# Kernel optimization log

Hardware: AMD Instinct MI355X
Metric: run time of the kernel (lower is better)

Reference implementation:

```python
import jax, jax.numpy as jnp
import numpy as np

N = 8192
IN, HID, NH, TOT = 64, 64, 4, 128
DH = TOT // NH  # 32


def setup_inputs() -> dict:
    key = jax.random.key(0)
    ks = jax.random.split(key, 8)
    s = 0.05
    return {
        "input": jax.random.normal(ks[0], (N, IN), jnp.float32),
        "hx": jax.random.normal(ks[1], (N, HID), jnp.float32),
        "Wq": jax.random.normal(ks[2], (NH, TOT, DH), jnp.float32) * s,
        "Wk": jax.random.normal(ks[3], (NH, TOT, DH), jnp.float32) * s,
        "Wr": jax.random.normal(ks[4], (TOT, HID), jnp.float32) * s,
        "br": jnp.zeros((HID,), jnp.float32),
        "Wz": jax.random.normal(ks[5], (TOT, HID), jnp.float32) * s,
        "bz": jnp.zeros((HID,), jnp.float32),
        "Wh": jax.random.normal(ks[6], (TOT, HID), jnp.float32) * s,
        "bh": jnp.zeros((HID,), jnp.float32),
    }


def _dyn_adj(x, Wq, Wk):
    # x: [N, T]; multi-head attention adjacency, averaged over heads -> [N, N]
    q = jnp.einsum('nt,htd->hnd', x, Wq)
    k = jnp.einsum('nt,htd->hnd', x, Wk)
    scores = jnp.einsum('hnd,hmd->hnm', q, k) / jnp.sqrt(jnp.float32(DH))
    return jnp.mean(jax.nn.softmax(scores, axis=-1), axis=0)  # [N, N]


def reference(input, hx, Wq, Wk, Wr, br, Wz, bz, Wh, bh):
    x = jnp.concatenate([input, hx], axis=1)          # [N, TOT]
    adj = _dyn_adj(x, Wq, Wk)                         # [N, N] row-stochastic
    ax = adj @ x                                      # shared adjacency application
    r = jax.nn.sigmoid(ax @ Wr + br)                  # [N, HID]
    z = jax.nn.sigmoid(ax @ Wz + bz)                  # [N, HID]
    x2 = jnp.concatenate([input, r * hx], axis=1)     # [N, TOT]
    h = jnp.tanh((adj @ x2) @ Wh + bh)                # [N, HID]
    return z * hx + (1.0 - z) * h
```

## Files before the change

kernel.cpp:

```cpp
#include <hip/hip_runtime.h>
#include <hip/hip_bf16.h>

#define NN 8192
#define TOTD 128
#define HIDD 64
#define NHEAD 4
#define DHD 32
#define NCQ 16
#define JPB (NN / 32 / NCQ)

typedef __attribute__((ext_vector_type(8))) short short8;
typedef __attribute__((ext_vector_type(4))) float f32x4;
typedef __attribute__((ext_vector_type(16))) float f32x16;

__device__ __forceinline__ short f2b(float f) {
  unsigned u = __builtin_bit_cast(unsigned, f);
  u += 0x7fff + ((u >> 16) & 1);
  return (short)(u >> 16);
}
__device__ __forceinline__ short f2b_fast(float f) {
  unsigned u = __builtin_bit_cast(unsigned, f);
  return (short)((u + 0x8000u) >> 16);
}
__device__ __forceinline__ float b2f(short s) {
  unsigned u = ((unsigned)(unsigned short)s) << 16;
  return __builtin_bit_cast(float, u);
}
__device__ __forceinline__ float fexp2(float x) {
#if __has_builtin(__builtin_amdgcn_exp2f)
  return __builtin_amdgcn_exp2f(x);
#else
  return exp2f(x);
#endif
}
__device__ __forceinline__ f32x16 zero16() {
  f32x16 z;
#pragma unroll
  for (int i = 0; i < 16; ++i) z[i] = 0.f;
  return z;
}


__global__ void k_build_xfrag(const float* __restrict__ in, const float* __restrict__ hx,
                              short* __restrict__ xb) {
  int i = blockIdx.x * 256 + threadIdx.x;
  int n = i >> 7;
  int t = i & 127;
  float v = (t < 64) ? in[n * 64 + t] : hx[n * 64 + (t - 64)];
  int jt = n >> 5, nn = n & 31;
  int m = nn >> 4, rem = nn & 15;
  int hi = (rem >> 2) & 1;
  int e = (rem & 3) | ((rem >> 3) << 2);
  int ct = t >> 5;
  int lane = (hi << 5) | (t & 31);
  xb[(((size_t)jt * 8 + ct * 2 + m) << 9) + (lane << 3) + e] = f2b(v);
}

__global__ __launch_bounds__(256, 2) void k_qk(
    const float* __restrict__ in, const float* __restrict__ hx,
    const float* __restrict__ Wq, const float* __restrict__ Wk,
    short* __restrict__ qb, short* __restrict__ kb) {
  __shared__ float Ws[32 * 256];
  __shared__ float xr_t[128 * 16];
  const int tid = threadIdx.x;
  const int n0 = blockIdx.x * 16;
  for (int i = tid; i < 2048; i += 256) {
    int r = i & 15, t = i >> 4;
    xr_t[t * 16 + r] = (t < 64) ? in[(n0 + r) * 64 + t] : hx[(n0 + r) * 64 + (t - 64)];
  }
  const int which = tid >> 7;
  const int h = (tid >> 5) & 3;
  const int d = tid & 31;
  const int c = tid;
  float acc[16];
#pragma unroll
  for (int r = 0; r < 16; ++r) acc[r] = 0.f;

  for (int pass = 0; pass < 4; ++pass) {
    __syncthreads();
    for (int i = tid; i < 32 * 256; i += 256) {
      int tt = pass * 32 + (i >> 8);
      int cc = i & 255;
      const float* W = (cc < 128) ? Wq : Wk;
      int hh = (cc >> 5) & 3, dd = cc & 31;
      Ws[(i >> 8) * 256 + cc] = W[((size_t)hh * 128 + tt) * 32 + dd];
    }
    __syncthreads();
#pragma unroll
    for (int t = 0; t < 32; ++t) {
      float wv = Ws[t * 256 + c];
      const float4* xp = (const float4*)&xr_t[(pass * 32 + t) * 16];
      float4 x0 = xp[0], x1 = xp[1], x2 = xp[2], x3 = xp[3];
      acc[0] += x0.x * wv;  acc[1] += x0.y * wv;  acc[2] += x0.z * wv;  acc[3] += x0.w * wv;
      acc[4] += x1.x * wv;  acc[5] += x1.y * wv;  acc[6] += x1.z * wv;  acc[7] += x1.w * wv;
      acc[8] += x2.x * wv;  acc[9] += x2.y * wv;  acc[10] += x2.z * wv; acc[11] += x2.w * wv;
      acc[12] += x3.x * wv; acc[13] += x3.y * wv; acc[14] += x3.z * wv; acc[15] += x3.w * wv;
    }
  }
#pragma unroll
  for (int r = 0; r < 16; ++r) {
    int n = n0 + r;
    int lane = (((d >> 3) & 1) << 5) | (n & 31);
    size_t idx = ((((size_t)(n >> 5) * 4 + h) * 2 + (d >> 4)) << 9) + (lane << 3) + (d & 7);
    if (which == 0) qb[idx] = f2b(acc[r] * 0.25503486f);
    else            kb[idx] = f2b(acc[r]);
  }
}

__global__ __launch_bounds__(256, 4) void k_denom(
    const short* __restrict__ qb, const short* __restrict__ kb,
    float* __restrict__ lpart_g) {
  const int tid = threadIdx.x;
  const int w = tid >> 6, l = tid & 63;
  const int r0 = blockIdx.x * 128 + w * 32;
  const int rt = blockIdx.x * 4 + w;
  const int jt0 = blockIdx.y * JPB;

  short8 qf[NHEAD][2];
#pragma unroll
  for (int h = 0; h < NHEAD; ++h)
#pragma unroll
    for (int m = 0; m < 2; ++m)
      qf[h][m] = *(const short8*)&qb[((((size_t)rt * 4 + h) * 2 + m) << 9) + l * 8];

  float acc[NHEAD] = {0.f, 0.f, 0.f, 0.f};

  for (int j = 0; j < JPB; ++j) {
    const short* kbase = kb + (((size_t)(jt0 + j) * 8) << 9) + l * 8;
#pragma unroll
    for (int h = 0; h < NHEAD; ++h) {
      short8 kf0 = *(const short8*)&kbase[(h * 2 + 0) << 9];
      short8 kf1 = *(const short8*)&kbase[(h * 2 + 1) << 9];
      f32x16 s = __builtin_amdgcn_mfma_f32_32x32x16_bf16(kf0, qf[h][0], zero16(), 0, 0, 0);
      s = __builtin_amdgcn_mfma_f32_32x32x16_bf16(kf1, qf[h][1], s, 0, 0, 0);
#pragma unroll
      for (int r = 0; r < 16; ++r) acc[h] += fexp2(s[r]);
    }
  }
#pragma unroll
  for (int h = 0; h < NHEAD; ++h) acc[h] += __shfl_xor(acc[h], 32, 64);
  if (l < 32) {
#pragma unroll
    for (int h = 0; h < NHEAD; ++h)
      lpart_g[((size_t)blockIdx.y * NHEAD + h) * NN + r0 + l] = acc[h];
  }
}

__global__ void k_linv(const float* __restrict__ lpart_g, float* __restrict__ linv_g) {
  int i = blockIdx.x * 256 + threadIdx.x;
  float s = 0.f;
#pragma unroll
  for (int q = 0; q < NCQ; ++q) s += lpart_g[(size_t)q * NHEAD * NN + i];
  linv_g[i] = 0.25f / s;
}

__global__ __launch_bounds__(256, 2) void k_pv1(
    const short* __restrict__ qb, const short* __restrict__ kb,
    const short* __restrict__ xb, const float* __restrict__ linv_g,
    short* __restrict__ axq, short* __restrict__ Pf, int storeP) {
  const int tid = threadIdx.x;
  const int w = tid >> 6, l = tid & 63;
  const int hi = l >> 5, col = l & 31;
  const int r0 = blockIdx.x * 128 + w * 32;
  const int rt = blockIdx.x * 4 + w;
  const int jt0 = blockIdx.y * JPB;

  short8 qf[NHEAD][2];
#pragma unroll
  for (int h = 0; h < NHEAD; ++h)
#pragma unroll
    for (int m = 0; m < 2; ++m)
      qf[h][m] = *(const short8*)&qb[((((size_t)rt * 4 + h) * 2 + m) << 9) + l * 8];
  float linv[NHEAD];
#pragma unroll
  for (int h = 0; h < NHEAD; ++h) linv[h] = linv_g[h * NN + r0 + col];

  f32x16 axa[4];
#pragma unroll
  for (int ct = 0; ct < 4; ++ct) axa[ct] = zero16();

  for (int j = 0; j < JPB; ++j) {
    const size_t jt = jt0 + j;
    const short* kbase = kb + ((jt * 8) << 9) + l * 8;
    const short* xbase = xb + ((jt * 8) << 9) + l * 8;
    short8 xv[8];
#pragma unroll
    for (int cchunk = 0; cchunk < 8; ++cchunk)
      xv[cchunk] = *(const short8*)&xbase[cchunk << 9];
    float p[16];
#pragma unroll
    for (int r = 0; r < 16; ++r) p[r] = 0.f;
#pragma unroll
    for (int h = 0; h < NHEAD; ++h) {
      short8 kf0 = *(const short8*)&kbase[(h * 2 + 0) << 9];
      short8 kf1 = *(const short8*)&kbase[(h * 2 + 1) << 9];
      f32x16 s = __builtin_amdgcn_mfma_f32_32x32x16_bf16(kf0, qf[h][0], zero16(), 0, 0, 0);
      s = __builtin_amdgcn_mfma_f32_32x32x16_bf16(kf1, qf[h][1], s, 0, 0, 0);
#pragma unroll
      for (int r = 0; r < 16; ++r) p[r] += fexp2(s[r]) * linv[h];
    }
    short8 pa0, pa1;
#pragma unroll
    for (int e = 0; e < 8; ++e) { pa0[e] = f2b_fast(p[e]); pa1[e] = f2b_fast(p[8 + e]); }
    if (storeP) {
      short8* pdst = (short8*)&Pf[(((size_t)rt * 256 + jt) << 10) + (l << 4)];
      pdst[0] = pa0;
      pdst[1] = pa1;
    }
#pragma unroll
    for (int ct = 0; ct < 4; ++ct) {
      axa[ct] = __builtin_amdgcn_mfma_f32_32x32x16_bf16(pa0, xv[ct * 2 + 0], axa[ct], 0, 0, 0);
      axa[ct] = __builtin_amdgcn_mfma_f32_32x32x16_bf16(pa1, xv[ct * 2 + 1], axa[ct], 0, 0, 0);
    }
  }
#pragma unroll
  for (int ct = 0; ct < 4; ++ct)
#pragma unroll
    for (int r = 0; r < 16; ++r) {
      int row = (r & 3) + 8 * (r >> 2) + 4 * hi;
      axq[(size_t)blockIdx.y * NN * TOTD + (size_t)(r0 + row) * TOTD + ct * 32 + col] =
          f2b(axa[ct][r]);
    }
}

__global__ __launch_bounds__(256) void k_rz(
    const short* __restrict__ axq, const float* __restrict__ hx,
    const float* __restrict__ Wr, const float* __restrict__ br,
    const float* __restrict__ Wz, const float* __restrict__ bz,
    float* __restrict__ ax, float* __restrict__ z, short* __restrict__ v2f) {
  __shared__ float axs[8][TOTD];
  const int tid = threadIdx.x;
  const int n0 = blockIdx.x * 8;
  for (int i = tid; i < 8 * TOTD; i += 256) {
    int rw = i >> 7, c = i & 127;
    int n = n0 + rw;
    float s = 0.f;
#pragma unroll
    for (int q = 0; q < NCQ; ++q) s += b2f(axq[((size_t)q * NN + n) * TOTD + c]);
    axs[rw][c] = s;
    if (c < 64) ax[(size_t)n * HIDD + c] = s;
  }
  __syncthreads();
  const int c2 = tid & 127;
  const int half = tid >> 7;
  const bool isz = c2 >= HIDD;
  const int c = c2 & (HIDD - 1);
  const float* W = isz ? Wz : Wr;
  const float bias = isz ? bz[c] : br[c];
  float a0 = bias, a1 = bias, a2 = bias, a3 = bias;
#pragma unroll
  for (int t = 0; t < TOTD; ++t) {
    float wv = W[t * HIDD + c];
    a0 += axs[half * 4 + 0][t] * wv;
    a1 += axs[half * 4 + 1][t] * wv;
    a2 += axs[half * 4 + 2][t] * wv;
    a3 += axs[half * 4 + 3][t] * wv;
  }
  float accs[4] = {a0, a1, a2, a3};
#pragma unroll
  for (int r = 0; r < 4; ++r) {
    int n = n0 + half * 4 + r;
    float sg = 1.f / (1.f + __expf(-accs[r]));
    if (isz) {
      z[(size_t)n * HIDD + c] = sg;
    } else {
      int jt = n >> 5, nn = n & 31;
      int m = nn >> 4, rem = nn & 15;
      int hh = (rem >> 2) & 1;
      int e = (rem & 3) | ((rem >> 3) << 2);
      int ct = c >> 5;
      int lane = (hh << 5) | (c & 31);
      v2f[(((size_t)jt * 4 + ct * 2 + m) << 9) + (lane << 3) + e] = f2b(sg * hx[(size_t)n * HIDD + c]);
    }
  }
}

__global__ __launch_bounds__(256, 8) void k_pv2P(
    const short* __restrict__ Pf, const short* __restrict__ v2f,
    short* __restrict__ a2q) {
  const int tid = threadIdx.x;
  const int w = tid >> 6, l = tid & 63;
  const int hi = l >> 5, col = l & 31;
  const int r0 = blockIdx.x * 128 + w * 32;
  const int rt = blockIdx.x * 4 + w;
  const int jt0 = blockIdx.y * JPB;

  f32x16 a2a[2];
#pragma unroll
  for (int ct = 0; ct < 2; ++ct) a2a[ct] = zero16();

  for (int j = 0; j < JPB; ++j) {
    const size_t jt = jt0 + j;
    const short8* pbase = (const short8*)&Pf[(((size_t)rt * 256 + jt) << 10) + (l << 4)];
    short8 pa0 = pbase[0];
    short8 pa1 = pbase[1];
    const short* vbase = v2f + ((jt * 4) << 9) + l * 8;
    short8 vv0 = *(const short8*)&vbase[0 << 9];
    short8 vv1 = *(const short8*)&vbase[1 << 9];
    short8 vv2 = *(const short8*)&vbase[2 << 9];
    short8 vv3 = *(const short8*)&vbase[3 << 9];
    a2a[0] = __builtin_amdgcn_mfma_f32_32x32x16_bf16(pa0, vv0, a2a[0], 0, 0, 0);
    a2a[0] = __builtin_amdgcn_mfma_f32_32x32x16_bf16(pa1, vv1, a2a[0], 0, 0, 0);
    a2a[1] = __builtin_amdgcn_mfma_f32_32x32x16_bf16(pa0, vv2, a2a[1], 0, 0, 0);
    a2a[1] = __builtin_amdgcn_mfma_f32_32x32x16_bf16(pa1, vv3, a2a[1], 0, 0, 0);
  }
#pragma unroll
  for (int ct = 0; ct < 2; ++ct)
#pragma unroll
    for (int r = 0; r < 16; ++r) {
      int row = (r & 3) + 8 * (r >> 2) + 4 * hi;
      a2q[(size_t)blockIdx.y * NN * HIDD + (size_t)(r0 + row) * HIDD + ct * 32 + col] =
          f2b(a2a[ct][r]);
    }
}

__global__ __launch_bounds__(256, 3) void k_pv2R(
    const short* __restrict__ qb, const short* __restrict__ kb,
    const short* __restrict__ v2f, const float* __restrict__ linv_g,
    short* __restrict__ a2q) {
  const int tid = threadIdx.x;
  const int w = tid >> 6, l = tid & 63;
  const int hi = l >> 5, col = l & 31;
  const int r0 = blockIdx.x * 128 + w * 32;
  const int rt = blockIdx.x * 4 + w;
  const int jt0 = blockIdx.y * JPB;

  short8 qf[NHEAD][2];
#pragma unroll
  for (int h = 0; h < NHEAD; ++h)
#pragma unroll
    for (int m = 0; m < 2; ++m)
      qf[h][m] = *(const short8*)&qb[((((size_t)rt * 4 + h) * 2 + m) << 9) + l * 8];
  float linv[NHEAD];
#pragma unroll
  for (int h = 0; h < NHEAD; ++h) linv[h] = linv_g[h * NN + r0 + col];

  f32x16 a2a[2];
#pragma unroll
  for (int ct = 0; ct < 2; ++ct) a2a[ct] = zero16();

  for (int j = 0; j < JPB; ++j) {
    const size_t jt = jt0 + j;
    const short* kbase = kb + ((jt * 8) << 9) + l * 8;
    const short* vbase = v2f + ((jt * 4) << 9) + l * 8;
    short8 vv0 = *(const short8*)&vbase[0 << 9];
    short8 vv1 = *(const short8*)&vbase[1 << 9];
    short8 vv2 = *(const short8*)&vbase[2 << 9];
    short8 vv3 = *(const short8*)&vbase[3 << 9];
    float p[16];
#pragma unroll
    for (int r = 0; r < 16; ++r) p[r] = 0.f;
#pragma unroll
    for (int h = 0; h < NHEAD; ++h) {
      short8 kf0 = *(const short8*)&kbase[(h * 2 + 0) << 9];
      short8 kf1 = *(const short8*)&kbase[(h * 2 + 1) << 9];
      f32x16 s = __builtin_amdgcn_mfma_f32_32x32x16_bf16(kf0, qf[h][0], zero16(), 0, 0, 0);
      s = __builtin_amdgcn_mfma_f32_32x32x16_bf16(kf1, qf[h][1], s, 0, 0, 0);
#pragma unroll
      for (int r = 0; r < 16; ++r) p[r] += fexp2(s[r]) * linv[h];
    }
    short8 pa0, pa1;
#pragma unroll
    for (int e = 0; e < 8; ++e) { pa0[e] = f2b_fast(p[e]); pa1[e] = f2b_fast(p[8 + e]); }
    a2a[0] = __builtin_amdgcn_mfma_f32_32x32x16_bf16(pa0, vv0, a2a[0], 0, 0, 0);
    a2a[0] = __builtin_amdgcn_mfma_f32_32x32x16_bf16(pa1, vv1, a2a[0], 0, 0, 0);
    a2a[1] = __builtin_amdgcn_mfma_f32_32x32x16_bf16(pa0, vv2, a2a[1], 0, 0, 0);
    a2a[1] = __builtin_amdgcn_mfma_f32_32x32x16_bf16(pa1, vv3, a2a[1], 0, 0, 0);
  }
#pragma unroll
  for (int ct = 0; ct < 2; ++ct)
#pragma unroll
    for (int r = 0; r < 16; ++r) {
      int row = (r & 3) + 8 * (r >> 2) + 4 * hi;
      a2q[(size_t)blockIdx.y * NN * HIDD + (size_t)(r0 + row) * HIDD + ct * 32 + col] =
          f2b(a2a[ct][r]);
    }
}

__global__ __launch_bounds__(256) void k_final(
    const short* __restrict__ a2q, const float* __restrict__ ax,
    const float* __restrict__ hx, const float* __restrict__ Wh,
    const float* __restrict__ bh, const float* __restrict__ z,
    float* __restrict__ out) {
  __shared__ float Whs[TOTD * HIDD];
  __shared__ float a2s[16][HIDD];
  const int tid = threadIdx.x;
  const int r0 = blockIdx.x * 16;

  for (int i = tid; i < TOTD * HIDD; i += 256) Whs[i] = Wh[i];
  for (int i = tid; i < 16 * HIDD; i += 256) {
    int rw = i >> 6, c = i & 63;
    size_t gi = (size_t)(r0 + rw) * HIDD + c;
    float s = 0.f;
#pragma unroll
    for (int q = 0; q < NCQ; ++q) s += b2f(a2q[(size_t)q * NN * HIDD + gi]);
    a2s[rw][c] = s;
  }
  __syncthreads();
  for (int o = tid; o < 16 * HIDD; o += 256) {
    int rw = o >> 6, c = o & 63;
    const float* axrow = &ax[(size_t)(r0 + rw) * HIDD];
    float acc = bh[c];
#pragma unroll
    for (int t = 0; t < 64; ++t) acc += axrow[t] * Whs[t * HIDD + c];
#pragma unroll
    for (int t = 0; t < 64; ++t) acc += a2s[rw][t] * Whs[(64 + t) * HIDD + c];
    float hval = tanhf(acc);
    size_t gi = (size_t)(r0 + rw) * HIDD + c;
    float zz = z[gi];
    out[gi] = zz * hx[gi] + (1.f - zz) * hval;
  }
}

extern "C" void kernel_launch(void* const* d_in, const int* in_sizes, int n_in,
                              void* d_out, int out_size, void* d_ws, size_t ws_size,
                              hipStream_t stream) {
  const float* in = (const float*)d_in[0];
  const float* hx = (const float*)d_in[1];
  const float* Wq = (const float*)d_in[2];
  const float* Wk = (const float*)d_in[3];
  const float* Wr = (const float*)d_in[4];
  const float* br = (const float*)d_in[5];
  const float* Wz = (const float*)d_in[6];
  const float* bz = (const float*)d_in[7];
  const float* Wh = (const float*)d_in[8];
  const float* bh = (const float*)d_in[9];

  const size_t MB = 1ull << 20;
  char* ws = (char*)d_ws;
  short* qb    = (short*)(ws + 0 * MB);
  short* kb    = (short*)(ws + 2 * MB);
  short* xb    = (short*)(ws + 4 * MB);
  float* linv  = (float*)(ws + 6 * MB);
  float* lpart = (float*)(ws + 6 * MB + 524288);
  float* ax    = (float*)(ws + 7 * MB);
  float* z     = (float*)(ws + 9 * MB);
  short* v2f   = (short*)(ws + 11 * MB);
  short* axq   = (short*)(ws + 12 * MB);
  short* a2q   = (short*)(ws + 44 * MB);
  short* Pf    = (short*)(ws + 60 * MB);
  float* out   = (float*)d_out;
  int useP = (ws_size >= 188 * MB) ? 1 : 0;

  k_build_xfrag<<<dim3((NN * TOTD) / 256), dim3(256), 0, stream>>>(in, hx, xb);
  k_qk<<<dim3(NN / 16), dim3(256), 0, stream>>>(in, hx, Wq, Wk, qb, kb);
  k_denom<<<dim3(NN / 128, NCQ), dim3(256), 0, stream>>>(qb, kb, lpart);
  k_linv<<<dim3((NHEAD * NN) / 256), dim3(256), 0, stream>>>(lpart, linv);
  k_pv1<<<dim3(NN / 128, NCQ), dim3(256), 0, stream>>>(qb, kb, xb, linv, axq, Pf, useP);
  k_rz<<<dim3(NN / 8), dim3(256), 0, stream>>>(axq, hx, Wr, br, Wz, bz, ax, z, v2f);
  if (useP)
    k_pv2P<<<dim3(NN / 128, NCQ), dim3(256), 0, stream>>>(Pf, v2f, a2q);
  else
    k_pv2R<<<dim3(NN / 128, NCQ), dim3(256), 0, stream>>>(qb, kb, v2f, linv, a2q);
  k_final<<<dim3(NN / 16), dim3(256), 0, stream>>>(a2q, ax, hx, Wh, bh, z, out);
}
```

Baseline: 205.4 us.

## Double-buffer K fragments in attention kernels and vectorize partial-sum reductions

In the denominator, P·x and P·v2 kernels, the K fragments for the next key tile are prefetched into a register double buffer while the current tile's MFMAs and exp run, and the j loop is fully unrolled. The partial-sum reductions in k_rz and k_final now load 8 bf16 values per thread with short8 vector loads instead of scalar loads. Launch-bound occupancy hints are lowered on several kernels to leave registers for the prefetch buffers. The goal is to hide global-load latency and cut load instruction count, at the cost of more register pressure and lower occupancy.

```diff
diff --git a/kernel.cpp b/kernel.cpp
--- a/kernel.cpp
+++ b/kernel.cpp
@@ -107,7 +107,7 @@
   }
 }
 
-__global__ __launch_bounds__(256, 4) void k_denom(
+__global__ __launch_bounds__(256, 3) void k_denom(
     const short* __restrict__ qb, const short* __restrict__ kb,
     float* __restrict__ lpart_g) {
   const int tid = threadIdx.x;
@@ -125,14 +125,23 @@
 
   float acc[NHEAD] = {0.f, 0.f, 0.f, 0.f};
 
+  short8 kf[2][8];
+#pragma unroll
+  for (int c = 0; c < 8; ++c)
+    kf[0][c] = *(const short8*)&kb[(((size_t)jt0 * 8 + c) << 9) + l * 8];
+
+#pragma unroll
   for (int j = 0; j < JPB; ++j) {
-    const short* kbase = kb + (((size_t)(jt0 + j) * 8) << 9) + l * 8;
+    const int cur = j & 1;
+    if (j + 1 < JPB) {
+#pragma unroll
+      for (int c = 0; c < 8; ++c)
+        kf[cur ^ 1][c] = *(const short8*)&kb[(((size_t)(jt0 + j + 1) * 8 + c) << 9) + l * 8];
+    }
 #pragma unroll
     for (int h = 0; h < NHEAD; ++h) {
-      short8 kf0 = *(const short8*)&kbase[(h * 2 + 0) << 9];
-      short8 kf1 = *(const short8*)&kbase[(h * 2 + 1) << 9];
-      f32x16 s = __builtin_amdgcn_mfma_f32_32x32x16_bf16(kf0, qf[h][0], zero16(), 0, 0, 0);
-      s = __builtin_amdgcn_mfma_f32_32x32x16_bf16(kf1, qf[h][1], s, 0, 0, 0);
+      f32x16 s = __builtin_amdgcn_mfma_f32_32x32x16_bf16(kf[cur][h * 2 + 0], qf[h][0], zero16(), 0, 0, 0);
+      s = __builtin_amdgcn_mfma_f32_32x32x16_bf16(kf[cur][h * 2 + 1], qf[h][1], s, 0, 0, 0);
 #pragma unroll
       for (int r = 0; r < 16; ++r) acc[h] += fexp2(s[r]);
     }
@@ -179,23 +188,32 @@
 #pragma unroll
   for (int ct = 0; ct < 4; ++ct) axa[ct] = zero16();
 
+  short8 kf[2][8];
+#pragma unroll
+  for (int c = 0; c < 8; ++c)
+    kf[0][c] = *(const short8*)&kb[(((size_t)jt0 * 8 + c) << 9) + l * 8];
+
+#pragma unroll
   for (int j = 0; j < JPB; ++j) {
+    const int cur = j & 1;
     const size_t jt = jt0 + j;
-    const short* kbase = kb + ((jt * 8) << 9) + l * 8;
     const short* xbase = xb + ((jt * 8) << 9) + l * 8;
     short8 xv[8];
 #pragma unroll
     for (int cchunk = 0; cchunk < 8; ++cchunk)
       xv[cchunk] = *(const short8*)&xbase[cchunk << 9];
+    if (j + 1 < JPB) {
+#pragma unroll
+      for (int c = 0; c < 8; ++c)
+        kf[cur ^ 1][c] = *(const short8*)&kb[(((size_t)(jt + 1) * 8 + c) << 9) + l * 8];
+    }
     float p[16];
 #pragma unroll
     for (int r = 0; r < 16; ++r) p[r] = 0.f;
 #pragma unroll
     for (int h = 0; h < NHEAD; ++h) {
-      short8 kf0 = *(const short8*)&kbase[(h * 2 + 0) << 9];
-      short8 kf1 = *(const short8*)&kbase[(h * 2 + 1) << 9];
-      f32x16 s = __builtin_amdgcn_mfma_f32_32x32x16_bf16(kf0, qf[h][0], zero16(), 0, 0, 0);
-      s = __builtin_amdgcn_mfma_f32_32x32x16_bf16(kf1, qf[h][1], s, 0, 0, 0);
+      f32x16 s = __builtin_amdgcn_mfma_f32_32x32x16_bf16(kf[cur][h * 2 + 0], qf[h][0], zero16(), 0, 0, 0);
+      s = __builtin_amdgcn_mfma_f32_32x32x16_bf16(kf[cur][h * 2 + 1], qf[h][1], s, 0, 0, 0);
 #pragma unroll
       for (int r = 0; r < 16; ++r) p[r] += fexp2(s[r]) * linv[h];
     }
@@ -223,7 +241,7 @@
     }
 }
 
-__global__ __launch_bounds__(256) void k_rz(
+__global__ __launch_bounds__(256, 2) void k_rz(
     const short* __restrict__ axq, const float* __restrict__ hx,
     const float* __restrict__ Wr, const float* __restrict__ br,
     const float* __restrict__ Wz, const float* __restrict__ bz,
@@ -231,14 +249,24 @@
   __shared__ float axs[8][TOTD];
   const int tid = threadIdx.x;
   const int n0 = blockIdx.x * 8;
-  for (int i = tid; i < 8 * TOTD; i += 256) {
-    int rw = i >> 7, c = i & 127;
-    int n = n0 + rw;
-    float s = 0.f;
-#pragma unroll
-    for (int q = 0; q < NCQ; ++q) s += b2f(axq[((size_t)q * NN + n) * TOTD + c]);
-    axs[rw][c] = s;
-    if (c < 64) ax[(size_t)n * HIDD + c] = s;
+  if (tid < 128) {
+    const int rw = tid >> 4, g = tid & 15;
+    const int n = n0 + rw;
+    float s[8];
+#pragma unroll
+    for (int e = 0; e < 8; ++e) s[e] = 0.f;
+#pragma unroll 4
+    for (int q = 0; q < NCQ; ++q) {
+      short8 v = *(const short8*)&axq[((size_t)q * NN + n) * TOTD + g * 8];
+#pragma unroll
+      for (int e = 0; e < 8; ++e) s[e] += b2f(v[e]);
+    }
+#pragma unroll
+    for (int e = 0; e < 8; ++e) axs[rw][g * 8 + e] = s[e];
+    if (g < 8) {
+#pragma unroll
+      for (int e = 0; e < 8; ++e) ax[(size_t)n * HIDD + g * 8 + e] = s[e];
+    }
   }
   __syncthreads();
   const int c2 = tid & 127;
@@ -275,7 +303,7 @@
   }
 }
 
-__global__ __launch_bounds__(256, 8) void k_pv2P(
+__global__ __launch_bounds__(256, 4) void k_pv2P(
     const short* __restrict__ Pf, const short* __restrict__ v2f,
     short* __restrict__ a2q) {
   const int tid = threadIdx.x;
@@ -289,6 +317,7 @@
 #pragma unroll
   for (int ct = 0; ct < 2; ++ct) a2a[ct] = zero16();
 
+#pragma unroll
   for (int j = 0; j < JPB; ++j) {
     const size_t jt = jt0 + j;
     const short8* pbase = (const short8*)&Pf[(((size_t)rt * 256 + jt) << 10) + (l << 4)];
@@ -339,23 +368,32 @@
 #pragma unroll
   for (int ct = 0; ct < 2; ++ct) a2a[ct] = zero16();
 
+  short8 kf[2][8];
+#pragma unroll
+  for (int c = 0; c < 8; ++c)
+    kf[0][c] = *(const short8*)&kb[(((size_t)jt0 * 8 + c) << 9) + l * 8];
+
+#pragma unroll
   for (int j = 0; j < JPB; ++j) {
+    const int cur = j & 1;
     const size_t jt = jt0 + j;
-    const short* kbase = kb + ((jt * 8) << 9) + l * 8;
     const short* vbase = v2f + ((jt * 4) << 9) + l * 8;
     short8 vv0 = *(const short8*)&vbase[0 << 9];
     short8 vv1 = *(const short8*)&vbase[1 << 9];
     short8 vv2 = *(const short8*)&vbase[2 << 9];
     short8 vv3 = *(const short8*)&vbase[3 << 9];
+    if (j + 1 < JPB) {
+#pragma unroll
+      for (int c = 0; c < 8; ++c)
+        kf[cur ^ 1][c] = *(const short8*)&kb[(((size_t)(jt + 1) * 8 + c) << 9) + l * 8];
+    }
     float p[16];
 #pragma unroll
     for (int r = 0; r < 16; ++r) p[r] = 0.f;
 #pragma unroll
     for (int h = 0; h < NHEAD; ++h) {
-      short8 kf0 = *(const short8*)&kbase[(h * 2 + 0) << 9];
-      short8 kf1 = *(const short8*)&kbase[(h * 2 + 1) << 9];
-      f32x16 s = __builtin_amdgcn_mfma_f32_32x32x16_bf16(kf0, qf[h][0], zero16(), 0, 0, 0);
-      s = __builtin_amdgcn_mfma_f32_32x32x16_bf16(kf1, qf[h][1], s, 0, 0, 0);
+      f32x16 s = __builtin_amdgcn_mfma_f32_32x32x16_bf16(kf[cur][h * 2 + 0], qf[h][0], zero16(), 0, 0, 0);
+      s = __builtin_amdgcn_mfma_f32_32x32x16_bf16(kf[cur][h * 2 + 1], qf[h][1], s, 0, 0, 0);
 #pragma unroll
       for (int r = 0; r < 16; ++r) p[r] += fexp2(s[r]) * linv[h];
     }
@@ -388,13 +426,19 @@
   const int r0 = blockIdx.x * 16;
 
   for (int i = tid; i < TOTD * HIDD; i += 256) Whs[i] = Wh[i];
-  for (int i = tid; i < 16 * HIDD; i += 256) {
-    int rw = i >> 6, c = i & 63;
-    size_t gi = (size_t)(r0 + rw) * HIDD + c;
-    float s = 0.f;
-#pragma unroll
-    for (int q = 0; q < NCQ; ++q) s += b2f(a2q[(size_t)q * NN * HIDD + gi]);
-    a2s[rw][c] = s;
+  if (tid < 128) {
+    const int rw = tid >> 3, g = tid & 7;
+    float s[8];
+#pragma unroll
+    for (int e = 0; e < 8; ++e) s[e] = 0.f;
+#pragma unroll 4
+    for (int q = 0; q < NCQ; ++q) {
+      short8 v = *(const short8*)&a2q[((size_t)q * NN + r0 + rw) * HIDD + g * 8];
+#pragma unroll
+      for (int e = 0; e < 8; ++e) s[e] += b2f(v[e]);
+    }
+#pragma unroll
+    for (int e = 0; e < 8; ++e) a2s[rw][g * 8 + e] = s[e];
   }
   __syncthreads();
   for (int o = tid; o < 16 * HIDD; o += 256) {
```

Result: slower. 369.9 us (+80.1%).
